# Performance work log

Hardware: AMD Instinct MI355X
Metric: run time of the kernel (lower is better)

Reference implementation:

```python
import jax, jax.numpy as jnp
import numpy as np

N = 20000   # nodes per node type
D = 128     # hidden_dim
H = 4       # num_heads
L = 2       # num_layers
E = 80000   # edges per relation


def setup_inputs() -> dict:
    key = jax.random.key(0)
    ks = jax.random.split(key, 24)
    w = lambda i, shape: jax.random.normal(ks[i], shape, dtype=jnp.float32) * 0.05
    ei = lambda i: jax.random.randint(ks[i], (2, E), 0, N, dtype=jnp.int32)
    return {
        'x_my': jax.random.normal(ks[0], (N, D), dtype=jnp.float32),
        'x_opp': jax.random.normal(ks[1], (N, D), dtype=jnp.float32),
        'gat_beats_Wl': w(2, (L, D, H * D)),
        'gat_beats_Wr': w(3, (L, D, H * D)),
        'gat_beats_att': w(4, (L, H, D)),
        'gat_beats_b': w(5, (L, D)),
        'gat_rev_Wl': w(6, (L, D, H * D)),
        'gat_rev_Wr': w(7, (L, D, H * D)),
        'gat_rev_att': w(8, (L, H, D)),
        'gat_rev_b': w(9, (L, D)),
        'cg_lose_Wf': w(10, (L, 2 * D, D)),
        'cg_lose_bf': w(11, (L, D)),
        'cg_lose_Ws': w(12, (L, 2 * D, D)),
        'cg_lose_bs': w(13, (L, D)),
        'cg_rev_Wf': w(14, (L, 2 * D, D)),
        'cg_rev_bf': w(15, (L, D)),
        'cg_rev_Ws': w(16, (L, 2 * D, D)),
        'cg_rev_bs': w(17, (L, D)),
        'nw_W': w(18, (L, D, D)),
        'nw_b': w(19, (L, D)),
        'ei_beats': ei(20),
        'ei_loses': ei(21),
        'ei_rev_beats': ei(22),
        'ei_rev_loses': ei(23),
    }


def _segment_softmax(scores, seg, num):
    # scores [E, H]; softmax over edges sharing the same destination node
    m = jax.ops.segment_max(scores, seg, num_segments=num)
    m = jnp.where(jnp.isfinite(m), m, 0.0)  # empty segments -> -inf guard
    e = jnp.exp(scores - m[seg])
    s = jax.ops.segment_sum(e, seg, num_segments=num)
    return e / (s[seg] + 1e-16)


def _gatv2(x_src, x_dst, src, dst, Wl, Wr, att, b, num_dst):
    # PyG GATv2Conv, heads=H, concat=False, add_self_loops=False
    xl = (x_src @ Wl).reshape(x_src.shape[0], H, D)  # [Ns, H, D]
    xr = (x_dst @ Wr).reshape(x_dst.shape[0], H, D)  # [Nd, H, D]
    z = jax.nn.leaky_relu(xl[src] + xr[dst], negative_slope=0.2)  # [E, H, D]
    score = jnp.einsum('ehd,hd->eh', z, att)
    alpha = _segment_softmax(score, dst, num_dst)
    out = jax.ops.segment_sum(xl[src] * alpha[:, :, None], dst, num_segments=num_dst)
    return out.mean(axis=1) + b  # concat=False -> mean over heads, then bias


def _cgconv(x_src, x_dst, src, dst, Wf, bf, Ws, bs, num_dst):
    # PyG CGConv: z = [x_i (dst), x_j (src)], gate * softplus, aggr='add', residual
    z = jnp.concatenate([x_dst[dst], x_src[src]], axis=-1)  # [E, 2D]
    m = jax.nn.sigmoid(z @ Wf + bf) * jax.nn.softplus(z @ Ws + bs)
    return jax.ops.segment_sum(m, dst, num_segments=num_dst) + x_dst


def reference(x_my, x_opp,
              gat_beats_Wl, gat_beats_Wr, gat_beats_att, gat_beats_b,
              gat_rev_Wl, gat_rev_Wr, gat_rev_att, gat_rev_b,
              cg_lose_Wf, cg_lose_bf, cg_lose_Ws, cg_lose_bs,
              cg_rev_Wf, cg_rev_bf, cg_rev_Ws, cg_rev_bs,
              nw_W, nw_b,
              ei_beats, ei_loses, ei_rev_beats, ei_rev_loses):
    for l in range(L):
        # HeteroConv with aggr='sum': sum per-relation outputs per dst node type
        opp_new = (_gatv2(x_my, x_opp, ei_beats[0], ei_beats[1],
                          gat_beats_Wl[l], gat_beats_Wr[l], gat_beats_att[l], gat_beats_b[l],
                          x_opp.shape[0])
                   + _cgconv(x_my, x_opp, ei_loses[0], ei_loses[1],
                             cg_lose_Wf[l], cg_lose_bf[l], cg_lose_Ws[l], cg_lose_bs[l],
                             x_opp.shape[0]))
        my_new = (_cgconv(x_opp, x_my, ei_rev_beats[0], ei_rev_beats[1],
                          cg_rev_Wf[l], cg_rev_bf[l], cg_rev_Ws[l], cg_rev_bs[l],
                          x_my.shape[0])
                  + _gatv2(x_opp, x_my, ei_rev_loses[0], ei_rev_loses[1],
                           gat_rev_Wl[l], gat_rev_Wr[l], gat_rev_att[l], gat_rev_b[l],
                           x_my.shape[0]))
        # shared nodewise Linear applied to every node type
        x_my = my_new @ nw_W[l] + nw_b[l]
        x_opp = opp_new @ nw_W[l] + nw_b[l]
    return x_my, x_opp
```

## Files before the change

kernel.cpp:

```cpp
#include <hip/hip_runtime.h>
#include <hip/hip_bf16.h>
#include <cstddef>

#define NNODE 20000
#define DDIM  128
#define NHEAD 4
#define NEDGE 80000

typedef __attribute__((ext_vector_type(8))) short short8;
typedef __attribute__((ext_vector_type(4))) short short4v;
typedef __attribute__((ext_vector_type(4))) float f32x4;

__device__ __forceinline__ float bf2f(unsigned short u) {
  union { unsigned u32; float f; } c; c.u32 = ((unsigned)u) << 16; return c.f;
}
__device__ __forceinline__ unsigned short f2bf(float f) {
  union { float f; unsigned u; } c; c.f = f;
  unsigned u = c.u;
  unsigned r = 0x7FFFu + ((u >> 16) & 1u);
  return (unsigned short)((u + r) >> 16);
}

template<typename AT, typename OutT>
__global__ __launch_bounds__(256, 2) void gemm_mfma(
    const AT* __restrict__ A0, const unsigned short* __restrict__ B0, OutT* __restrict__ C0,
    const AT* __restrict__ A1, const unsigned short* __restrict__ B1, OutT* __restrict__ C1,
    int halfY, int M, int N, const float* __restrict__ bias)
{
  __shared__ unsigned short As[128 * 128];
  __shared__ unsigned short Bs[128 * 128];
  int by = blockIdx.y;
  const AT* A = A0; const unsigned short* Bt = B0; OutT* C = C0;
  if (by >= halfY) { by -= halfY; A = A1; Bt = B1; C = C1; }
  const int bm = by * 128;
  const int bn = blockIdx.x * 128;
  const int t  = threadIdx.x;
  char* asb = (char*)As;
  char* bsb = (char*)Bs;

  if constexpr (sizeof(AT) == 4) {
    #pragma unroll
    for (int i = 0; i < 16; ++i) {
      int e = i * 1024 + t * 4;
      int r = e >> 7, c = e & 127;
      float4 v = make_float4(0.f, 0.f, 0.f, 0.f);
      if (bm + r < M) v = *reinterpret_cast<const float4*>((const float*)A + (size_t)(bm + r) * 128 + c);
      short4v h;
      h.x = (short)f2bf(v.x); h.y = (short)f2bf(v.y);
      h.z = (short)f2bf(v.z); h.w = (short)f2bf(v.w);
      *reinterpret_cast<short4v*>(asb + r * 256 + ((c * 2) ^ ((r & 7) << 4))) = h;
    }
  } else {
    const char* atile = (const char*)((const unsigned short*)A + (size_t)bm * 128);
    #pragma unroll
    for (int i = 0; i < 8; ++i) {
      int fo = i * 4096 + t * 16;
      int r = fo >> 8, boff = fo & 255;
      short8 v = {0, 0, 0, 0, 0, 0, 0, 0};
      if (bm + r < M) v = *reinterpret_cast<const short8*>(atile + fo);
      *reinterpret_cast<short8*>(asb + r * 256 + (boff ^ ((r & 7) << 4))) = v;
    }
  }
  const char* btile = (const char*)(Bt + (size_t)bn * 128);
  #pragma unroll
  for (int i = 0; i < 8; ++i) {
    int fo = i * 4096 + t * 16;
    int r = fo >> 8, boff = fo & 255;
    short8 v = *reinterpret_cast<const short8*>(btile + fo);
    *reinterpret_cast<short8*>(bsb + r * 256 + (boff ^ ((r & 7) << 4))) = v;
  }
  __syncthreads();

  const int w  = t >> 6;
  const int wr = w >> 1, wc = w & 1;
  const int lane = t & 63;
  const int l15 = lane & 15, lg = lane >> 4;

  f32x4 acc[4][4];
  #pragma unroll
  for (int m = 0; m < 4; ++m)
    #pragma unroll
    for (int n = 0; n < 4; ++n) acc[m][n] = (f32x4){0.f, 0.f, 0.f, 0.f};

  #pragma unroll
  for (int kk = 0; kk < 4; ++kk) {
    const int kbyte = (kk * 32 + lg * 8) * 2;
    short8 af[4], bfr[4];
    #pragma unroll
    for (int m = 0; m < 4; ++m) {
      int r = wr * 64 + m * 16 + l15;
      af[m] = *reinterpret_cast<const short8*>(asb + r * 256 + (kbyte ^ ((r & 7) << 4)));
    }
    #pragma unroll
    for (int n = 0; n < 4; ++n) {
      int r = wc * 64 + n * 16 + l15;
      bfr[n] = *reinterpret_cast<const short8*>(bsb + r * 256 + (kbyte ^ ((r & 7) << 4)));
    }
    #pragma unroll
    for (int m = 0; m < 4; ++m)
      #pragma unroll
      for (int n = 0; n < 4; ++n)
        acc[m][n] = __builtin_amdgcn_mfma_f32_16x16x32_bf16(af[m], bfr[n], acc[m][n], 0, 0, 0);
  }

  #pragma unroll
  for (int m = 0; m < 4; ++m) {
    #pragma unroll
    for (int j = 0; j < 4; ++j) {
      int row = bm + wr * 64 + m * 16 + lg * 4 + j;
      if (row >= M) continue;
      #pragma unroll
      for (int n = 0; n < 4; ++n) {
        int col = bn + wc * 64 + n * 16 + l15;
        float v = acc[m][n][j];
        if (bias) v += bias[col];
        if constexpr (sizeof(OutT) == 2) {
          C[(size_t)row * N + col] = (OutT)f2bf(v);
        } else {
          C[(size_t)row * N + col] = v;
        }
      }
    }
  }
}

__global__ __launch_bounds__(256) void pack_gat(
    const float* __restrict__ gbWl, const float* __restrict__ gbWr,
    const float* __restrict__ grWl, const float* __restrict__ grWr,
    unsigned short* __restrict__ out)
{
  int idx = blockIdx.x * 256 + threadIdx.x;
  if (idx >= 2 * 2 * 1024 * 128) return;
  int k = idx & 127;
  int n = (idx >> 7) & 1023;
  int type = (idx >> 17) & 1;
  int l = idx >> 18;
  const float* W; int col;
  if (type == 0) { if (n < 512) { W = gbWl; col = n; } else { W = grWr; col = n - 512; } }
  else           { if (n < 512) { W = gbWr; col = n; } else { W = grWl; col = n - 512; } }
  out[idx] = f2bf(W[(size_t)l * 128 * 512 + (size_t)k * 512 + col]);
}

__global__ __launch_bounds__(256) void pack_cg(
    const float* __restrict__ clWf, const float* __restrict__ clWs,
    const float* __restrict__ crWf, const float* __restrict__ crWs,
    unsigned short* __restrict__ out)
{
  int idx = blockIdx.x * 256 + threadIdx.x;
  if (idx >= 2 * 2 * 512 * 128) return;
  int k = idx & 127;
  int n = (idx >> 7) & 511;
  int type = (idx >> 16) & 1;
  int l = idx >> 17;
  int blk = n >> 7, c = n & 127;
  const float* W; int row;
  if (type == 0) {
    if (blk == 0) { W = clWf; row = 128 + k; }
    else if (blk == 1) { W = clWs; row = 128 + k; }
    else if (blk == 2) { W = crWf; row = k; }
    else { W = crWs; row = k; }
  } else {
    if (blk == 0) { W = clWf; row = k; }
    else if (blk == 1) { W = clWs; row = k; }
    else if (blk == 2) { W = crWf; row = 128 + k; }
    else { W = crWs; row = 128 + k; }
  }
  out[idx] = f2bf(W[(size_t)l * 256 * 128 + (size_t)row * 128 + c]);
}

__global__ __launch_bounds__(256) void pack_nw(
    const float* __restrict__ nwW, unsigned short* __restrict__ out)
{
  int idx = blockIdx.x * 256 + threadIdx.x;
  if (idx >= 2 * 128 * 128) return;
  int k = idx & 127;
  int n = (idx >> 7) & 127;
  int l = idx >> 14;
  out[idx] = f2bf(nwW[(size_t)l * 128 * 128 + (size_t)k * 128 + n]);
}

__global__ __launch_bounds__(256) void f2b_kernel(
    const float* __restrict__ in, unsigned short* __restrict__ out, int n)
{
  int idx = (blockIdx.x * 256 + threadIdx.x) * 8;
  if (idx >= n) return;
  float4 a = *reinterpret_cast<const float4*>(in + idx);
  float4 b = *reinterpret_cast<const float4*>(in + idx + 4);
  short8 o;
  o[0] = (short)f2bf(a.x); o[1] = (short)f2bf(a.y);
  o[2] = (short)f2bf(a.z); o[3] = (short)f2bf(a.w);
  o[4] = (short)f2bf(b.x); o[5] = (short)f2bf(b.y);
  o[6] = (short)f2bf(b.z); o[7] = (short)f2bf(b.w);
  *reinterpret_cast<short8*>(out + idx) = o;
}

__global__ __launch_bounds__(256) void build_buckets(
    const int* __restrict__ e0, const int* __restrict__ e1,
    const int* __restrict__ e2, const int* __restrict__ e3,
    unsigned* __restrict__ cnt, int* __restrict__ bucket)
{
  int idx = blockIdx.x * 256 + threadIdx.x;
  if (idx >= 4 * NEDGE) return;
  int set = idx / NEDGE;
  int e = idx - set * NEDGE;
  const int* ei = (set == 0) ? e0 : (set == 1) ? e1 : (set == 2) ? e2 : e3;
  int s = ei[e], d = ei[NEDGE + e];
  unsigned slot = atomicAdd(&cnt[set * NNODE + d], 1u);
  if (slot < 64u) bucket[((size_t)set * NNODE + d) * 64 + slot] = s;
}

__global__ __launch_bounds__(256) void gat_csr(
    const unsigned short* __restrict__ xl, const unsigned short* __restrict__ xr,
    const unsigned short* __restrict__ xres,
    const int* __restrict__ bucket, const unsigned* __restrict__ cnt,
    const float* __restrict__ att, const float* __restrict__ bias,
    float* __restrict__ acc)
{
  int d = blockIdx.x * 4 + (threadIdx.x >> 6);
  int lane = threadIdx.x & 63;
  int h = lane >> 4, q = lane & 15;
  unsigned n = cnt[d]; n = (n > 64u) ? 64u : n;

  short8 xrv = *reinterpret_cast<const short8*>(xr + (size_t)d * 1024 + h * 128 + q * 8);
  float4 at0 = *reinterpret_cast<const float4*>(att + h * 128 + q * 8);
  float4 at1 = *reinterpret_cast<const float4*>(att + h * 128 + q * 8 + 4);
  float xrf[8], atf[8];
  atf[0] = at0.x; atf[1] = at0.y; atf[2] = at0.z; atf[3] = at0.w;
  atf[4] = at1.x; atf[5] = at1.y; atf[6] = at1.z; atf[7] = at1.w;
  #pragma unroll
  for (int j = 0; j < 8; ++j) xrf[j] = bf2f((unsigned short)xrv[j]);

  float uout[8] = {0.f, 0.f, 0.f, 0.f, 0.f, 0.f, 0.f, 0.f};
  float ssum = 0.f;
  const int* bk = bucket + (size_t)d * 64;
  for (unsigned i = 0; i < n; ++i) {
    int s = bk[i];
    short8 xlv = *reinterpret_cast<const short8*>(xl + (size_t)s * 1024 + h * 128 + q * 8);
    float xlf[8];
    #pragma unroll
    for (int j = 0; j < 8; ++j) xlf[j] = bf2f((unsigned short)xlv[j]);
    float sum = 0.f;
    #pragma unroll
    for (int j = 0; j < 8; ++j) {
      float z = xlf[j] + xrf[j];
      z = (z > 0.f) ? z : 0.2f * z;
      sum += atf[j] * z;
    }
    #pragma unroll
    for (int m = 1; m < 16; m <<= 1) sum += __shfl_xor(sum, m);
    float e = __expf(fminf(sum, 80.f));
    ssum += e;
    #pragma unroll
    for (int j = 0; j < 8; ++j) uout[j] += e * xlf[j];
  }
  float scale = __builtin_amdgcn_rcpf(ssum + 1e-16f) * 0.25f;
  #pragma unroll
  for (int j = 0; j < 8; ++j) {
    float v = uout[j] * scale;
    v += __shfl_xor(v, 16);
    v += __shfl_xor(v, 32);
    uout[j] = v;
  }
  if (h == 0) {
    short8 xs = *reinterpret_cast<const short8*>(xres + (size_t)d * 128 + q * 8);
    const float* bp = bias + q * 8;
    float4 o0, o1;
    o0.x = uout[0] + bf2f((unsigned short)xs[0]) + bp[0];
    o0.y = uout[1] + bf2f((unsigned short)xs[1]) + bp[1];
    o0.z = uout[2] + bf2f((unsigned short)xs[2]) + bp[2];
    o0.w = uout[3] + bf2f((unsigned short)xs[3]) + bp[3];
    o1.x = uout[4] + bf2f((unsigned short)xs[4]) + bp[4];
    o1.y = uout[5] + bf2f((unsigned short)xs[5]) + bp[5];
    o1.z = uout[6] + bf2f((unsigned short)xs[6]) + bp[6];
    o1.w = uout[7] + bf2f((unsigned short)xs[7]) + bp[7];
    *reinterpret_cast<float4*>(acc + (size_t)d * 128 + q * 8) = o0;
    *reinterpret_cast<float4*>(acc + (size_t)d * 128 + q * 8 + 4) = o1;
  }
}

__global__ __launch_bounds__(256) void cg_csr(
    const unsigned short* __restrict__ Fd, const unsigned short* __restrict__ Fs,
    const unsigned short* __restrict__ Sd, const unsigned short* __restrict__ Ss,
    const int* __restrict__ bucket, const unsigned* __restrict__ cnt,
    const float* __restrict__ bf_, const float* __restrict__ bs_,
    float* __restrict__ acc)
{
  int d = blockIdx.x * 4 + (threadIdx.x >> 6);
  unsigned n = cnt[d]; n = (n > 64u) ? 64u : n;
  if (n == 0) return;
  int lane = threadIdx.x & 63;
  int c0 = lane * 2;
  unsigned fdu = *reinterpret_cast<const unsigned*>(Fd + (size_t)d * 512 + c0);
  unsigned sdu = *reinterpret_cast<const unsigned*>(Sd + (size_t)d * 512 + c0);
  float fd0 = bf2f((unsigned short)(fdu & 0xffffu)) + bf_[c0];
  float fd1 = bf2f((unsigned short)(fdu >> 16))     + bf_[c0 + 1];
  float sd0 = bf2f((unsigned short)(sdu & 0xffffu)) + bs_[c0];
  float sd1 = bf2f((unsigned short)(sdu >> 16))     + bs_[c0 + 1];
  float a0 = 0.f, a1 = 0.f;
  const int* bk = bucket + (size_t)d * 64;
  for (unsigned i = 0; i < n; ++i) {
    int s = bk[i];
    unsigned fsu = *reinterpret_cast<const unsigned*>(Fs + (size_t)s * 512 + c0);
    unsigned ssu = *reinterpret_cast<const unsigned*>(Ss + (size_t)s * 512 + c0);
    float g0 = fd0 + bf2f((unsigned short)(fsu & 0xffffu));
    float g1 = fd1 + bf2f((unsigned short)(fsu >> 16));
    float t0 = sd0 + bf2f((unsigned short)(ssu & 0xffffu));
    float t1 = sd1 + bf2f((unsigned short)(ssu >> 16));
    float gate0 = __builtin_amdgcn_rcpf(1.f + __expf(-g0));
    float gate1 = __builtin_amdgcn_rcpf(1.f + __expf(-g1));
    float sp0 = fmaxf(t0, 0.f) + __logf(1.f + __expf(-fabsf(t0)));
    float sp1 = fmaxf(t1, 0.f) + __logf(1.f + __expf(-fabsf(t1)));
    a0 += gate0 * sp0;
    a1 += gate1 * sp1;
  }
  float2 v = *reinterpret_cast<float2*>(acc + (size_t)d * 128 + c0);
  v.x += a0; v.y += a1;
  *reinterpret_cast<float2*>(acc + (size_t)d * 128 + c0) = v;
}


extern "C" void kernel_launch(void* const* d_in, const int* in_sizes, int n_in,
                              void* d_out, int out_size, void* d_ws, size_t ws_size,
                              hipStream_t stream) {
  const float* x_my_in  = (const float*)d_in[0];
  const float* x_opp_in = (const float*)d_in[1];
  const float* gb_Wl  = (const float*)d_in[2];
  const float* gb_Wr  = (const float*)d_in[3];
  const float* gb_att = (const float*)d_in[4];
  const float* gb_b   = (const float*)d_in[5];
  const float* gr_Wl  = (const float*)d_in[6];
  const float* gr_Wr  = (const float*)d_in[7];
  const float* gr_att = (const float*)d_in[8];
  const float* gr_b   = (const float*)d_in[9];
  const float* cl_Wf  = (const float*)d_in[10];
  const float* cl_bf  = (const float*)d_in[11];
  const float* cl_Ws  = (const float*)d_in[12];
  const float* cl_bs  = (const float*)d_in[13];
  const float* cr_Wf  = (const float*)d_in[14];
  const float* cr_bf  = (const float*)d_in[15];
  const float* cr_Ws  = (const float*)d_in[16];
  const float* cr_bs  = (const float*)d_in[17];
  const float* nw_W   = (const float*)d_in[18];
  const float* nw_b   = (const float*)d_in[19];
  const int* ei_beats     = (const int*)d_in[20];
  const int* ei_loses     = (const int*)d_in[21];
  const int* ei_rev_beats = (const int*)d_in[22];
  const int* ei_rev_loses = (const int*)d_in[23];

  float* out = (float*)d_out;

  const size_t ND = (size_t)NNODE * DDIM;
  unsigned short* XAb = (unsigned short*)d_ws;
  float* NM  = (float*)(XAb + 2 * ND);
  float* NO  = NM + ND;
  unsigned short* PJM = (unsigned short*)(NM + 2 * ND);
  unsigned short* PJO = PJM + (size_t)NNODE * 1024;
  unsigned* CNT = (unsigned*)(PJO + (size_t)NNODE * 1024);
  int* BKT = (int*)(CNT + 4 * NNODE);
  unsigned short* PKG = (unsigned short*)(BKT + (size_t)4 * NNODE * 64);
  unsigned short* PKC = PKG + 2 * 2 * 1024 * 128;
  unsigned short* PKN = PKC + 2 * 2 * 512 * 128;

  const int cvb = (int)(ND / 8 + 255) / 256;
  const int nwb = NNODE / 4;

  hipLaunchKernelGGL(pack_gat, dim3(2 * 2 * 1024 * 128 / 256), dim3(256), 0, stream,
                     gb_Wl, gb_Wr, gr_Wl, gr_Wr, PKG);
  hipLaunchKernelGGL(pack_cg, dim3(2 * 2 * 512 * 128 / 256), dim3(256), 0, stream,
                     cl_Wf, cl_Ws, cr_Wf, cr_Ws, PKC);
  hipLaunchKernelGGL(pack_nw, dim3(2 * 128 * 128 / 256), dim3(256), 0, stream, nw_W, PKN);

  hipLaunchKernelGGL(f2b_kernel, dim3(cvb), dim3(256), 0, stream, x_my_in,  XAb,      (int)ND);
  hipLaunchKernelGGL(f2b_kernel, dim3(cvb), dim3(256), 0, stream, x_opp_in, XAb + ND, (int)ND);

  hipMemsetAsync(CNT, 0, 4 * NNODE * sizeof(unsigned), stream);
  hipLaunchKernelGGL(build_buckets, dim3((4 * NEDGE + 255) / 256), dim3(256), 0, stream,
                     ei_beats, ei_rev_loses, ei_loses, ei_rev_beats, CNT, BKT);

  for (int l = 0; l < 2; ++l) {
    const size_t oA = (size_t)l * NHEAD * DDIM;
    const size_t oB = (size_t)l * DDIM;

    hipLaunchKernelGGL((gemm_mfma<unsigned short, unsigned short>), dim3(8, 314), dim3(256), 0, stream,
                       XAb,      PKG + (size_t)(l * 2 + 0) * 1024 * 128, PJM,
                       XAb + ND, PKG + (size_t)(l * 2 + 1) * 1024 * 128, PJO,
                       157, NNODE, 1024, (const float*)nullptr);

    hipLaunchKernelGGL(gat_csr, dim3(nwb), dim3(256), 0, stream,
                       PJM, PJO, XAb + ND, BKT + (size_t)0 * NNODE * 64, CNT + 0 * NNODE,
                       gb_att + oA, gb_b + oB, NO);
    hipLaunchKernelGGL(gat_csr, dim3(nwb), dim3(256), 0, stream,
                       PJO + 512, PJM + 512, XAb, BKT + (size_t)1 * NNODE * 64, CNT + 1 * NNODE,
                       gr_att + oA, gr_b + oB, NM);

    hipLaunchKernelGGL((gemm_mfma<unsigned short, unsigned short>), dim3(4, 314), dim3(256), 0, stream,
                       XAb,      PKC + (size_t)(l * 2 + 0) * 512 * 128, PJM,
                       XAb + ND, PKC + (size_t)(l * 2 + 1) * 512 * 128, PJO,
                       157, NNODE, 512, (const float*)nullptr);

    hipLaunchKernelGGL(cg_csr, dim3(nwb), dim3(256), 0, stream,
                       PJO + 0, PJM + 0, PJO + 128, PJM + 128,
                       BKT + (size_t)2 * NNODE * 64, CNT + 2 * NNODE,
                       cl_bf + oB, cl_bs + oB, NO);
    hipLaunchKernelGGL(cg_csr, dim3(nwb), dim3(256), 0, stream,
                       PJM + 256, PJO + 256, PJM + 384, PJO + 384,
                       BKT + (size_t)3 * NNODE * 64, CNT + 3 * NNODE,
                       cr_bf + oB, cr_bs + oB, NM);

    if (l == 0) {
      hipLaunchKernelGGL((gemm_mfma<float, unsigned short>), dim3(1, 313), dim3(256), 0, stream,
                         NM, PKN + (size_t)l * 128 * 128, XAb,
                         NM, PKN + (size_t)l * 128 * 128, XAb,
                         313, 2 * NNODE, 128, nw_b + oB);
    } else {
      hipLaunchKernelGGL((gemm_mfma<float, float>), dim3(1, 313), dim3(256), 0, stream,
                         NM, PKN + (size_t)l * 128 * 128, out,
                         NM, PKN + (size_t)l * 128 * 128, out,
                         313, 2 * NNODE, 128, nw_b + oB);
    }
  }
  (void)in_sizes; (void)n_in; (void)out_size; (void)ws_size;
}
```

Measured before the change: 480.2 us.

## Fuse GAT and CGConv edge kernels, stream A from global in GEMM

Merges the two GAT and two CGConv aggregation kernels into one launch per layer that handles both node types and writes each output once, so the read-modify-write pass over the accumulator goes away. The GAT and CG neighbour loops now prefetch the next source row, and the CG loop splits edges across the four head groups. The GEMM drops its A tile from shared memory and loads A fragments straight from global, raises occupancy to 4 blocks, and remaps workgroup IDs across 8 XCDs. CG projections get their own buffers so both GEMMs can run before the fused kernel, at the cost of more workspace and possibly redundant global A reads.

```diff
diff --git a/kernel.cpp b/kernel.cpp
--- a/kernel.cpp
+++ b/kernel.cpp
@@ -8,7 +8,6 @@
 #define NEDGE 80000
 
 typedef __attribute__((ext_vector_type(8))) short short8;
-typedef __attribute__((ext_vector_type(4))) short short4v;
 typedef __attribute__((ext_vector_type(4))) float f32x4;
 
 __device__ __forceinline__ float bf2f(unsigned short u) {
@@ -22,45 +21,26 @@
 }
 
 template<typename AT, typename OutT>
-__global__ __launch_bounds__(256, 2) void gemm_mfma(
+__global__ __launch_bounds__(256, 4) void gemm_mfma(
     const AT* __restrict__ A0, const unsigned short* __restrict__ B0, OutT* __restrict__ C0,
     const AT* __restrict__ A1, const unsigned short* __restrict__ B1, OutT* __restrict__ C1,
     int halfY, int M, int N, const float* __restrict__ bias)
 {
-  __shared__ unsigned short As[128 * 128];
   __shared__ unsigned short Bs[128 * 128];
-  int by = blockIdx.y;
+  const int nwgx = gridDim.x;
+  const int nwg = nwgx * gridDim.y;
+  int orig = blockIdx.x + nwgx * blockIdx.y;
+  int q8 = nwg >> 3, r8 = nwg & 7;
+  int xc = orig & 7, lo = orig >> 3;
+  int wg = ((xc < r8) ? xc * (q8 + 1) : r8 * (q8 + 1) + (xc - r8) * q8) + lo;
+  int by = wg / nwgx;
+  int bx = wg - by * nwgx;
   const AT* A = A0; const unsigned short* Bt = B0; OutT* C = C0;
   if (by >= halfY) { by -= halfY; A = A1; Bt = B1; C = C1; }
-  const int bm = by * 128;
-  const int bn = blockIdx.x * 128;
-  const int t  = threadIdx.x;
-  char* asb = (char*)As;
+  const int bm = by * 128, bn = bx * 128;
+  const int t = threadIdx.x;
   char* bsb = (char*)Bs;
 
-  if constexpr (sizeof(AT) == 4) {
-    #pragma unroll
-    for (int i = 0; i < 16; ++i) {
-      int e = i * 1024 + t * 4;
-      int r = e >> 7, c = e & 127;
-      float4 v = make_float4(0.f, 0.f, 0.f, 0.f);
-      if (bm + r < M) v = *reinterpret_cast<const float4*>((const float*)A + (size_t)(bm + r) * 128 + c);
-      short4v h;
-      h.x = (short)f2bf(v.x); h.y = (short)f2bf(v.y);
-      h.z = (short)f2bf(v.z); h.w = (short)f2bf(v.w);
-      *reinterpret_cast<short4v*>(asb + r * 256 + ((c * 2) ^ ((r & 7) << 4))) = h;
-    }
-  } else {
-    const char* atile = (const char*)((const unsigned short*)A + (size_t)bm * 128);
-    #pragma unroll
-    for (int i = 0; i < 8; ++i) {
-      int fo = i * 4096 + t * 16;
-      int r = fo >> 8, boff = fo & 255;
-      short8 v = {0, 0, 0, 0, 0, 0, 0, 0};
-      if (bm + r < M) v = *reinterpret_cast<const short8*>(atile + fo);
-      *reinterpret_cast<short8*>(asb + r * 256 + (boff ^ ((r & 7) << 4))) = v;
-    }
-  }
   const char* btile = (const char*)(Bt + (size_t)bn * 128);
   #pragma unroll
   for (int i = 0; i < 8; ++i) {
@@ -71,10 +51,9 @@
   }
   __syncthreads();
 
-  const int w  = t >> 6;
-  const int wr = w >> 1, wc = w & 1;
-  const int lane = t & 63;
-  const int l15 = lane & 15, lg = lane >> 4;
+  const int w = t >> 6, wr = w >> 1, wc = w & 1;
+  const int lane = t & 63, l15 = lane & 15, lg = lane >> 4;
+  const int rowl = bm + wr * 64 + l15;
 
   f32x4 acc[4][4];
   #pragma unroll
@@ -84,13 +63,26 @@
 
   #pragma unroll
   for (int kk = 0; kk < 4; ++kk) {
-    const int kbyte = (kk * 32 + lg * 8) * 2;
+    const int kb = kk * 32 + lg * 8;
     short8 af[4], bfr[4];
     #pragma unroll
     for (int m = 0; m < 4; ++m) {
-      int r = wr * 64 + m * 16 + l15;
-      af[m] = *reinterpret_cast<const short8*>(asb + r * 256 + (kbyte ^ ((r & 7) << 4)));
-    }
+      if constexpr (sizeof(AT) == 4) {
+        const float* ap = (const float*)A + ((size_t)(rowl + m * 16) << 7) + kb;
+        float4 v0 = *reinterpret_cast<const float4*>(ap);
+        float4 v1 = *reinterpret_cast<const float4*>(ap + 4);
+        short8 hv;
+        hv[0] = (short)f2bf(v0.x); hv[1] = (short)f2bf(v0.y);
+        hv[2] = (short)f2bf(v0.z); hv[3] = (short)f2bf(v0.w);
+        hv[4] = (short)f2bf(v1.x); hv[5] = (short)f2bf(v1.y);
+        hv[6] = (short)f2bf(v1.z); hv[7] = (short)f2bf(v1.w);
+        af[m] = hv;
+      } else {
+        af[m] = *reinterpret_cast<const short8*>(
+            (const unsigned short*)A + ((size_t)(rowl + m * 16) << 7) + kb);
+      }
+    }
+    const int kbyte = kb * 2;
     #pragma unroll
     for (int n = 0; n < 4; ++n) {
       int r = wc * 64 + n * 16 + l15;
@@ -209,18 +201,51 @@
   if (slot < 64u) bucket[((size_t)set * NNODE + d) * 64 + slot] = s;
 }
 
-__global__ __launch_bounds__(256) void gat_csr(
-    const unsigned short* __restrict__ xl, const unsigned short* __restrict__ xr,
-    const unsigned short* __restrict__ xres,
-    const int* __restrict__ bucket, const unsigned* __restrict__ cnt,
-    const float* __restrict__ att, const float* __restrict__ bias,
-    float* __restrict__ acc)
-{
-  int d = blockIdx.x * 4 + (threadIdx.x >> 6);
+__global__ __launch_bounds__(256) void edge_fused(
+    const unsigned short* __restrict__ xlA, const unsigned short* __restrict__ xrA,
+    const unsigned short* __restrict__ FsA, const unsigned short* __restrict__ SsA,
+    const unsigned short* __restrict__ FdA, const unsigned short* __restrict__ SdA,
+    const unsigned short* __restrict__ xresA,
+    const int* __restrict__ bgA, const unsigned* __restrict__ cgA,
+    const int* __restrict__ bcA, const unsigned* __restrict__ ccA,
+    const float* __restrict__ attA, const float* __restrict__ biasA,
+    const float* __restrict__ bfA, const float* __restrict__ bsA,
+    float* __restrict__ accA,
+    const unsigned short* __restrict__ xlB, const unsigned short* __restrict__ xrB,
+    const unsigned short* __restrict__ FsB, const unsigned short* __restrict__ SsB,
+    const unsigned short* __restrict__ FdB, const unsigned short* __restrict__ SdB,
+    const unsigned short* __restrict__ xresB,
+    const int* __restrict__ bgB, const unsigned* __restrict__ cgB,
+    const int* __restrict__ bcB, const unsigned* __restrict__ ccB,
+    const float* __restrict__ attB, const float* __restrict__ biasB,
+    const float* __restrict__ bfB, const float* __restrict__ bsB,
+    float* __restrict__ accB, int nwb)
+{
+  int blk = blockIdx.x;
+  int second = (blk >= nwb) ? 1 : 0;
+  if (second) blk -= nwb;
+  int d = blk * 4 + (threadIdx.x >> 6);
   int lane = threadIdx.x & 63;
   int h = lane >> 4, q = lane & 15;
-  unsigned n = cnt[d]; n = (n > 64u) ? 64u : n;
-
+
+  const unsigned short* xl  = second ? xlB  : xlA;
+  const unsigned short* xr  = second ? xrB  : xrA;
+  const unsigned short* Fs  = second ? FsB  : FsA;
+  const unsigned short* Ss  = second ? SsB  : SsA;
+  const unsigned short* Fd  = second ? FdB  : FdA;
+  const unsigned short* Sd  = second ? SdB  : SdA;
+  const unsigned short* xres = second ? xresB : xresA;
+  const int* bg = second ? bgB : bgA;
+  const unsigned* cg = second ? cgB : cgA;
+  const int* bc = second ? bcB : bcA;
+  const unsigned* cc = second ? ccB : ccA;
+  const float* att  = second ? attB  : attA;
+  const float* bias = second ? biasB : biasA;
+  const float* bf_  = second ? bfB   : bfA;
+  const float* bs_  = second ? bsB   : bsA;
+  float* acc = second ? accB : accA;
+
+  unsigned ng = cg[d]; ng = (ng > 64u) ? 64u : ng;
   short8 xrv = *reinterpret_cast<const short8*>(xr + (size_t)d * 1024 + h * 128 + q * 8);
   float4 at0 = *reinterpret_cast<const float4*>(att + h * 128 + q * 8);
   float4 at1 = *reinterpret_cast<const float4*>(att + h * 128 + q * 8 + 4);
@@ -232,10 +257,18 @@
 
   float uout[8] = {0.f, 0.f, 0.f, 0.f, 0.f, 0.f, 0.f, 0.f};
   float ssum = 0.f;
-  const int* bk = bucket + (size_t)d * 64;
-  for (unsigned i = 0; i < n; ++i) {
-    int s = bk[i];
-    short8 xlv = *reinterpret_cast<const short8*>(xl + (size_t)s * 1024 + h * 128 + q * 8);
+  const int* bkg = bg + (size_t)d * 64;
+  short8 xln = {0,0,0,0,0,0,0,0};
+  if (ng > 0) {
+    int s0 = bkg[0];
+    xln = *reinterpret_cast<const short8*>(xl + (size_t)s0 * 1024 + h * 128 + q * 8);
+  }
+  for (unsigned i = 0; i < ng; ++i) {
+    short8 xlv = xln;
+    if (i + 1 < ng) {
+      int s2 = bkg[i + 1];
+      xln = *reinterpret_cast<const short8*>(xl + (size_t)s2 * 1024 + h * 128 + q * 8);
+    }
     float xlf[8];
     #pragma unroll
     for (int j = 0; j < 8; ++j) xlf[j] = bf2f((unsigned short)xlv[j]);
@@ -261,61 +294,68 @@
     v += __shfl_xor(v, 32);
     uout[j] = v;
   }
+
+  unsigned nc = cc[d]; nc = (nc > 64u) ? 64u : nc;
+  float fd[8], sd[8], ac[8];
+  {
+    short8 fdv = *reinterpret_cast<const short8*>(Fd + (size_t)d * 512 + q * 8);
+    short8 sdv = *reinterpret_cast<const short8*>(Sd + (size_t)d * 512 + q * 8);
+    const float* bfp = bf_ + q * 8;
+    const float* bsp = bs_ + q * 8;
+    #pragma unroll
+    for (int j = 0; j < 8; ++j) {
+      fd[j] = bf2f((unsigned short)fdv[j]) + bfp[j];
+      sd[j] = bf2f((unsigned short)sdv[j]) + bsp[j];
+      ac[j] = 0.f;
+    }
+  }
+  const int* bkc = bc + (size_t)d * 64;
+  short8 fsn = {0,0,0,0,0,0,0,0}, ssn = {0,0,0,0,0,0,0,0};
+  unsigned i0 = (unsigned)h;
+  if (i0 < nc) {
+    int s0 = bkc[i0];
+    fsn = *reinterpret_cast<const short8*>(Fs + (size_t)s0 * 512 + q * 8);
+    ssn = *reinterpret_cast<const short8*>(Ss + (size_t)s0 * 512 + q * 8);
+  }
+  for (unsigned i = i0; i < nc; i += 4) {
+    short8 fsv = fsn, ssv = ssn;
+    if (i + 4 < nc) {
+      int s2 = bkc[i + 4];
+      fsn = *reinterpret_cast<const short8*>(Fs + (size_t)s2 * 512 + q * 8);
+      ssn = *reinterpret_cast<const short8*>(Ss + (size_t)s2 * 512 + q * 8);
+    }
+    #pragma unroll
+    for (int j = 0; j < 8; ++j) {
+      float g  = fd[j] + bf2f((unsigned short)fsv[j]);
+      float tt = sd[j] + bf2f((unsigned short)ssv[j]);
+      float gate = __builtin_amdgcn_rcpf(1.f + __expf(-g));
+      float sp = fmaxf(tt, 0.f) + __logf(1.f + __expf(-fabsf(tt)));
+      ac[j] += gate * sp;
+    }
+  }
+  #pragma unroll
+  for (int j = 0; j < 8; ++j) {
+    float v = ac[j];
+    v += __shfl_xor(v, 16);
+    v += __shfl_xor(v, 32);
+    ac[j] = v;
+  }
+
   if (h == 0) {
     short8 xs = *reinterpret_cast<const short8*>(xres + (size_t)d * 128 + q * 8);
     const float* bp = bias + q * 8;
     float4 o0, o1;
-    o0.x = uout[0] + bf2f((unsigned short)xs[0]) + bp[0];
-    o0.y = uout[1] + bf2f((unsigned short)xs[1]) + bp[1];
-    o0.z = uout[2] + bf2f((unsigned short)xs[2]) + bp[2];
-    o0.w = uout[3] + bf2f((unsigned short)xs[3]) + bp[3];
-    o1.x = uout[4] + bf2f((unsigned short)xs[4]) + bp[4];
-    o1.y = uout[5] + bf2f((unsigned short)xs[5]) + bp[5];
-    o1.z = uout[6] + bf2f((unsigned short)xs[6]) + bp[6];
-    o1.w = uout[7] + bf2f((unsigned short)xs[7]) + bp[7];
+    o0.x = uout[0] + ac[0] + bf2f((unsigned short)xs[0]) + bp[0];
+    o0.y = uout[1] + ac[1] + bf2f((unsigned short)xs[1]) + bp[1];
+    o0.z = uout[2] + ac[2] + bf2f((unsigned short)xs[2]) + bp[2];
+    o0.w = uout[3] + ac[3] + bf2f((unsigned short)xs[3]) + bp[3];
+    o1.x = uout[4] + ac[4] + bf2f((unsigned short)xs[4]) + bp[4];
+    o1.y = uout[5] + ac[5] + bf2f((unsigned short)xs[5]) + bp[5];
+    o1.z = uout[6] + ac[6] + bf2f((unsigned short)xs[6]) + bp[6];
+    o1.w = uout[7] + ac[7] + bf2f((unsigned short)xs[7]) + bp[7];
     *reinterpret_cast<float4*>(acc + (size_t)d * 128 + q * 8) = o0;
     *reinterpret_cast<float4*>(acc + (size_t)d * 128 + q * 8 + 4) = o1;
   }
-}
-
-__global__ __launch_bounds__(256) void cg_csr(
-    const unsigned short* __restrict__ Fd, const unsigned short* __restrict__ Fs,
-    const unsigned short* __restrict__ Sd, const unsigned short* __restrict__ Ss,
-    const int* __restrict__ bucket, const unsigned* __restrict__ cnt,
-    const float* __restrict__ bf_, const float* __restrict__ bs_,
-    float* __restrict__ acc)
-{
-  int d = blockIdx.x * 4 + (threadIdx.x >> 6);
-  unsigned n = cnt[d]; n = (n > 64u) ? 64u : n;
-  if (n == 0) return;
-  int lane = threadIdx.x & 63;
-  int c0 = lane * 2;
-  unsigned fdu = *reinterpret_cast<const unsigned*>(Fd + (size_t)d * 512 + c0);
-  unsigned sdu = *reinterpret_cast<const unsigned*>(Sd + (size_t)d * 512 + c0);
-  float fd0 = bf2f((unsigned short)(fdu & 0xffffu)) + bf_[c0];
-  float fd1 = bf2f((unsigned short)(fdu >> 16))     + bf_[c0 + 1];
-  float sd0 = bf2f((unsigned short)(sdu & 0xffffu)) + bs_[c0];
-  float sd1 = bf2f((unsigned short)(sdu >> 16))     + bs_[c0 + 1];
-  float a0 = 0.f, a1 = 0.f;
-  const int* bk = bucket + (size_t)d * 64;
-  for (unsigned i = 0; i < n; ++i) {
-    int s = bk[i];
-    unsigned fsu = *reinterpret_cast<const unsigned*>(Fs + (size_t)s * 512 + c0);
-    unsigned ssu = *reinterpret_cast<const unsigned*>(Ss + (size_t)s * 512 + c0);
-    float g0 = fd0 + bf2f((unsigned short)(fsu & 0xffffu));
-    float g1 = fd1 + bf2f((unsigned short)(fsu >> 16));
-    float t0 = sd0 + bf2f((unsigned short)(ssu & 0xffffu));
-    float t1 = sd1 + bf2f((unsigned short)(ssu >> 16));
-    float gate0 = __builtin_amdgcn_rcpf(1.f + __expf(-g0));
-    float gate1 = __builtin_amdgcn_rcpf(1.f + __expf(-g1));
-    float sp0 = fmaxf(t0, 0.f) + __logf(1.f + __expf(-fabsf(t0)));
-    float sp1 = fmaxf(t1, 0.f) + __logf(1.f + __expf(-fabsf(t1)));
-    a0 += gate0 * sp0;
-    a1 += gate1 * sp1;
-  }
-  float2 v = *reinterpret_cast<float2*>(acc + (size_t)d * 128 + c0);
-  v.x += a0; v.y += a1;
-  *reinterpret_cast<float2*>(acc + (size_t)d * 128 + c0) = v;
 }
 
 
@@ -355,7 +395,9 @@
   float* NO  = NM + ND;
   unsigned short* PJM = (unsigned short*)(NM + 2 * ND);
   unsigned short* PJO = PJM + (size_t)NNODE * 1024;
-  unsigned* CNT = (unsigned*)(PJO + (size_t)NNODE * 1024);
+  unsigned short* PCM = PJO + (size_t)NNODE * 1024;
+  unsigned short* PCO = PCM + (size_t)NNODE * 512;
+  unsigned* CNT = (unsigned*)(PCO + (size_t)NNODE * 512);
   int* BKT = (int*)(CNT + 4 * NNODE);
   unsigned short* PKG = (unsigned short*)(BKT + (size_t)4 * NNODE * 64);
   unsigned short* PKC = PKG + 2 * 2 * 1024 * 128;
@@ -386,26 +428,25 @@
                        XAb + ND, PKG + (size_t)(l * 2 + 1) * 1024 * 128, PJO,
                        157, NNODE, 1024, (const float*)nullptr);
 
-    hipLaunchKernelGGL(gat_csr, dim3(nwb), dim3(256), 0, stream,
-                       PJM, PJO, XAb + ND, BKT + (size_t)0 * NNODE * 64, CNT + 0 * NNODE,
-                       gb_att + oA, gb_b + oB, NO);
-    hipLaunchKernelGGL(gat_csr, dim3(nwb), dim3(256), 0, stream,
-                       PJO + 512, PJM + 512, XAb, BKT + (size_t)1 * NNODE * 64, CNT + 1 * NNODE,
-                       gr_att + oA, gr_b + oB, NM);
-
     hipLaunchKernelGGL((gemm_mfma<unsigned short, unsigned short>), dim3(4, 314), dim3(256), 0, stream,
-                       XAb,      PKC + (size_t)(l * 2 + 0) * 512 * 128, PJM,
-                       XAb + ND, PKC + (size_t)(l * 2 + 1) * 512 * 128, PJO,
+                       XAb,      PKC + (size_t)(l * 2 + 0) * 512 * 128, PCM,
+                       XAb + ND, PKC + (size_t)(l * 2 + 1) * 512 * 128, PCO,
                        157, NNODE, 512, (const float*)nullptr);
 
-    hipLaunchKernelGGL(cg_csr, dim3(nwb), dim3(256), 0, stream,
-                       PJO + 0, PJM + 0, PJO + 128, PJM + 128,
+    hipLaunchKernelGGL(edge_fused, dim3(2 * nwb), dim3(256), 0, stream,
+                        PJM, PJO,
+                        PCM, PCM + 128, PCO, PCO + 128,
+                        XAb + ND,
+                       BKT + (size_t)0 * NNODE * 64, CNT + 0 * NNODE,
                        BKT + (size_t)2 * NNODE * 64, CNT + 2 * NNODE,
-                       cl_bf + oB, cl_bs + oB, NO);
-    hipLaunchKernelGGL(cg_csr, dim3(nwb), dim3(256), 0, stream,
-                       PJM + 256, PJO + 256, PJM + 384, PJO + 384,
+                       gb_att + oA, gb_b + oB, cl_bf + oB, cl_bs + oB, NO,
+                        PJO + 512, PJM + 512,
+                        PCO + 256, PCO + 384, PCM + 256, PCM + 384,
+                        XAb,
+                       BKT + (size_t)1 * NNODE * 64, CNT + 1 * NNODE,
                        BKT + (size_t)3 * NNODE * 64, CNT + 3 * NNODE,
-                       cr_bf + oB, cr_bs + oB, NM);
+                       gr_att + oA, gr_b + oB, cr_bf + oB, cr_bs + oB, NM,
+                       nwb);
 
     if (l == 0) {
       hipLaunchKernelGGL((gemm_mfma<float, unsigned short>), dim3(1, 313), dim3(256), 0, stream,
```

Measured after the change: 439.8 us. -8.4%, faster.
